# Performance work log

Hardware: AMD Instinct MI355X
Metric: run time of the kernel (lower is better)

Reference implementation:

```python
import jax, jax.numpy as jnp
import numpy as np

B, N, H, W = 2, 65536, 256, 256
FEA, OUT, CMP, MAX_PT = 8, 512, 32, 64
EPS = 1e-5


def _xavier(key, fan_in, fan_out):
    scale = np.sqrt(2.0 / (fan_in + fan_out)).astype(np.float32)
    return jax.random.normal(key, (fan_in, fan_out), dtype=jnp.float32) * scale


def setup_inputs() -> dict:
    key = jax.random.key(0)
    ks = jax.random.split(key, 8)
    pt_fea = jax.random.normal(ks[0], (B, N, FEA), dtype=jnp.float32)
    xy_ind = jax.random.randint(ks[1], (B, N, 2), 0, H, dtype=jnp.int32)
    return {
        "pt_fea": pt_fea,
        "bn0_g": jnp.ones((FEA,), jnp.float32), "bn0_b": jnp.zeros((FEA,), jnp.float32),
        "W1": _xavier(ks[2], FEA, 64),
        "bn1_g": jnp.ones((64,), jnp.float32), "bn1_b": jnp.zeros((64,), jnp.float32),
        "W2": _xavier(ks[3], 64, 128),
        "bn2_g": jnp.ones((128,), jnp.float32), "bn2_b": jnp.zeros((128,), jnp.float32),
        "W3": _xavier(ks[4], 128, 256),
        "bn3_g": jnp.ones((256,), jnp.float32), "bn3_b": jnp.zeros((256,), jnp.float32),
        "W4": _xavier(ks[5], 256, OUT),
        "Wc": _xavier(ks[6], OUT, CMP),
        "xy_ind": xy_ind,
    }


def _forward(pt_fea, bn0_g, bn0_b, W1, bn1_g, bn1_b, W2, bn2_g, bn2_b,
             W3, bn3_g, bn3_b, W4, Wc, xy_ind):
    Bc, Nc, Fc = pt_fea.shape
    P = Bc * Nc
    feats = pt_fea.reshape(P, Fc)
    batch_id = jnp.repeat(jnp.arange(Bc, dtype=jnp.int32), Nc)
    xy = xy_ind.reshape(P, 2)
    keys = batch_id * (H * W) + xy[:, 0] * W + xy[:, 1]  # linearized voxel id

    # random shuffle of points (torch.randperm)
    perm = jax.random.permutation(jax.random.key(42), P)
    feats = feats[perm]
    keys = keys[perm]

    # rank of each point within its voxel, in shuffled order
    # (== grp_range_torch(unq_cnt)[argsort(argsort(unq_inv))])
    order = jnp.argsort(keys)  # stable
    sk = keys[order]
    pos = jnp.arange(P)
    new_grp = jnp.concatenate([jnp.array([True]), sk[1:] != sk[:-1]])
    grp_start = jax.lax.cummax(jnp.where(new_grp, pos, 0))
    rank = jnp.zeros(P, jnp.int32).at[order].set((pos - grp_start).astype(jnp.int32))
    mask = rank < MAX_PT  # keep at most MAX_PT points per voxel

    # PPmodel: BN -> Lin -> BN -> ReLU x3 -> Lin, BN stats over kept points only
    m = mask[:, None].astype(feats.dtype)
    cnt = jnp.sum(m)

    def bn(x, g, b):
        mu = jnp.sum(x * m, axis=0) / cnt
        var = jnp.sum(jnp.square(x - mu) * m, axis=0) / cnt  # biased var
        return (x - mu) * jax.lax.rsqrt(var + EPS) * g + b

    x = bn(feats, bn0_g, bn0_b)
    x = jax.nn.relu(bn(x @ W1, bn1_g, bn1_b))
    x = jax.nn.relu(bn(x @ W2, bn2_g, bn2_b))
    x = jax.nn.relu(bn(x @ W3, bn3_g, bn3_b))
    x = x @ W4  # [P, OUT]

    # scatter_max segment reduction into dense voxel grid
    NEG = jnp.finfo(x.dtype).min
    x = jnp.where(mask[:, None], x, NEG)
    S = Bc * H * W
    pooled = jax.ops.segment_max(x, keys, num_segments=S)
    occupied = jax.ops.segment_sum(jnp.ones(P, x.dtype), keys, num_segments=S) > 0
    pooled = jnp.where(occupied[:, None], pooled, 0.0)

    comp = jax.nn.relu(pooled @ Wc)  # fea_compression
    comp = jnp.where(occupied[:, None], comp, 0.0)  # empty voxels stay zero
    out = comp.reshape(Bc, H, W, CMP).transpose(0, 3, 1, 2)  # [B, C, H, W]
    return out


def reference(pt_fea, bn0_g, bn0_b, W1, bn1_g, bn1_b, W2, bn2_g, bn2_b,
              W3, bn3_g, bn3_b, W4, Wc, xy_ind):
    return _forward(pt_fea, bn0_g, bn0_b, W1, bn1_g, bn1_b, W2, bn2_g, bn2_b,
                    W3, bn3_g, bn3_b, W4, Wc, xy_ind)
```

## Files before the change

### kernel.cpp

```cpp
#include <hip/hip_runtime.h>
#include <cstdint>
#include <cstddef>


#define P_TOT  131072
#define HWSZ   65536
#define WGRID  256
#define S_TOT  131072
#define EPS    1e-5f
#define CNTF   131072.0f

#define OFF_Y3    0ull
#define OFF_Y1    67108864ull
#define OFF_Y2    100663296ull
#define OFF_POOL  67108864ull
#define OFF_CNT   201326592ull
#define OFF_ST    201850880ull
#define OFF_OFFS  201916416ull
#define OFF_CUR   202440704ull
#define OFF_BSUM  202964992ull
#define OFF_PIDF  202969088ull
#define OFF_SEND  203493376ull
#define OFF_SKEY  204017664ull
#define OFF_W3F   204541952ull
#define OFF_W4F   204607488ull
#define OFF_WCF   204869632ull
#define OFF_W2F   204902400ull
#define OFF_SCSH  204918784ull

typedef __attribute__((ext_vector_type(8)))  short bf16x8;
typedef __attribute__((ext_vector_type(16))) float f32x16;

__device__ __forceinline__ unsigned f2bf(float f) {
    unsigned u = __float_as_uint(f);
    return (u + 0x7FFFu + ((u >> 16) & 1u)) >> 16;
}
__device__ __forceinline__ float bf2f(unsigned h) {
    return __uint_as_float(h << 16);
}

__global__ __launch_bounds__(256) void k_zero(uint4* __restrict__ p, int n_u4) {
    int i = blockIdx.x * blockDim.x + threadIdx.x;
    if (i < n_u4) p[i] = make_uint4(0u, 0u, 0u, 0u);
}

__global__ __launch_bounds__(256) void k_prepw(
    const float* __restrict__ W2, const float* __restrict__ W3,
    const float* __restrict__ W4, const float* __restrict__ Wc,
    uint4* __restrict__ W2F, uint4* __restrict__ W3F,
    uint4* __restrict__ W4F, uint4* __restrict__ WcF)
{
    int gw = (blockIdx.x * 256 + threadIdx.x) >> 6;
    int l = threadIdx.x & 63;
    const float* W; uint4* dst; int M, mt, ks, fi;
    if (gw < 64)       { fi = gw;       W = W3; dst = W3F; M = 256; mt = fi >> 3; ks = fi & 7;  }
    else if (gw < 320) { fi = gw - 64;  W = W4; dst = W4F; M = 512; mt = fi >> 4; ks = fi & 15; }
    else if (gw < 352) { fi = gw - 320; W = Wc; dst = WcF; M = 32;  mt = 0;      ks = fi;      }
    else               { fi = gw - 352; W = W2; dst = W2F; M = 128; mt = fi >> 2; ks = fi & 3;  }
    int m = mt * 32 + (l & 31);
    int k0 = ks * 16 + (l >> 5) * 8;
    unsigned p[4];
    #pragma unroll
    for (int jj = 0; jj < 4; ++jj) {
        unsigned lo = f2bf(W[(size_t)(k0 + 2*jj)     * M + m]);
        unsigned hi = f2bf(W[(size_t)(k0 + 2*jj + 1) * M + m]);
        p[jj] = lo | (hi << 16);
    }
    dst[(size_t)fi * 64 + l] = make_uint4(p[0], p[1], p[2], p[3]);
}

__global__ __launch_bounds__(256) void k_bnprep(
    const float* __restrict__ st, const float* __restrict__ g,
    const float* __restrict__ b, float* __restrict__ sc,
    float* __restrict__ sh, int nch)
{
    int c = blockIdx.x * 256 + threadIdx.x;
    if (c >= nch) return;
    float mu = st[c * 16] * (1.0f / CNTF);
    float var = st[(nch + c) * 16] * (1.0f / CNTF) - mu * mu;
    float rs = rsqrtf(var + EPS);
    float s = rs * g[c];
    sc[c] = s;
    sh[c] = b[c] - mu * s;
}

__global__ __launch_bounds__(256) void k_fold(
    unsigned short* __restrict__ y, const float* __restrict__ sc,
    const float* __restrict__ sh, int nch, int n_u4)
{
    int i = blockIdx.x * 256 + threadIdx.x;
    if (i >= n_u4) return;
    int ch0 = (i * 8) & (nch - 1);
    float4 s0 = *(const float4*)(sc + ch0), s1 = *(const float4*)(sc + ch0 + 4);
    float4 h0 = *(const float4*)(sh + ch0), h1 = *(const float4*)(sh + ch0 + 4);
    float scv[8] = {s0.x,s0.y,s0.z,s0.w,s1.x,s1.y,s1.z,s1.w};
    float shv[8] = {h0.x,h0.y,h0.z,h0.w,h1.x,h1.y,h1.z,h1.w};
    uint4 e = ((const uint4*)y)[i];
    unsigned eu[4] = {e.x, e.y, e.z, e.w};
    unsigned ou[4];
    #pragma unroll
    for (int jj = 0; jj < 4; ++jj) {
        float x0 = fmaxf(fmaf(bf2f(eu[jj] & 0xFFFFu), scv[2*jj],   shv[2*jj]),   0.f);
        float x1 = fmaxf(fmaf(bf2f(eu[jj] >> 16),     scv[2*jj+1], shv[2*jj+1]), 0.f);
        ou[jj] = f2bf(x0) | (f2bf(x1) << 16);
    }
    ((uint4*)y)[i] = make_uint4(ou[0], ou[1], ou[2], ou[3]);
}

__global__ __launch_bounds__(256) void k_stats0(
    const float* __restrict__ pt, const int* __restrict__ xy,
    float* __restrict__ st0, unsigned* __restrict__ counts)
{
    __shared__ float part[4][16];
    const int tid = threadIdx.x;
    const int p = blockIdx.x * 256 + tid;
    const float4* f4 = (const float4*)(pt + (size_t)p * 8);
    float4 a = f4[0], b = f4[1];
    float v[8] = {a.x,a.y,a.z,a.w,b.x,b.y,b.z,b.w};
    int key = (p >> 16) * HWSZ + xy[2*p] * WGRID + xy[2*p + 1];
    atomicAdd(&counts[key], 1u);
    float s[8], q[8];
    #pragma unroll
    for (int k = 0; k < 8; ++k) { s[k] = v[k]; q[k] = v[k]*v[k]; }
    #pragma unroll
    for (int k = 0; k < 8; ++k) {
        #pragma unroll
        for (int off = 32; off > 0; off >>= 1) {
            s[k] += __shfl_down(s[k], off);
            q[k] += __shfl_down(q[k], off);
        }
    }
    if ((tid & 63) == 0) {
        int w = tid >> 6;
        #pragma unroll
        for (int k = 0; k < 8; ++k) { part[w][k] = s[k]; part[w][8 + k] = q[k]; }
    }
    __syncthreads();
    if (tid < 16) {
        float t = part[0][tid] + part[1][tid] + part[2][tid] + part[3][tid];
        atomicAdd(&st0[tid * 16], t);
    }
}

__global__ __launch_bounds__(256) void k_lin1(
    const float* __restrict__ pt, const float* __restrict__ g0,
    const float* __restrict__ b0, const float* __restrict__ W1,
    const float* __restrict__ st0, float* __restrict__ y1,
    float* __restrict__ st1)
{
    __shared__ float x0s[64 * 8];
    __shared__ float w1s[8 * 64];
    __shared__ float sc0s[8], sh0s[8];
    __shared__ float red[256];
    const int tid = threadIdx.x;

    if (tid < 8) {
        float mu = st0[tid * 16] * (1.0f / CNTF);
        float var = st0[(8 + tid) * 16] * (1.0f / CNTF) - mu * mu;
        float rs = rsqrtf(var + EPS);
        sc0s[tid] = rs * g0[tid];
        sh0s[tid] = b0[tid] - mu * rs * g0[tid];
    }
    if (tid < 128) ((float4*)w1s)[tid] = ((const float4*)W1)[tid];
    const int c = tid & 63;
    const int psub = tid >> 6;
    float ssum = 0.f, ssq = 0.f;
    for (int t = 0; t < 4; ++t) {
        const int pbase = blockIdx.x * 256 + t * 64;
        __syncthreads();
        if (tid < 128) {
            float4 f = ((const float4*)(pt + (size_t)pbase * 8))[tid];
            int cc = (tid & 1) * 4;
            f.x = fmaf(f.x, sc0s[cc + 0], sh0s[cc + 0]);
            f.y = fmaf(f.y, sc0s[cc + 1], sh0s[cc + 1]);
            f.z = fmaf(f.z, sc0s[cc + 2], sh0s[cc + 2]);
            f.w = fmaf(f.w, sc0s[cc + 3], sh0s[cc + 3]);
            ((float4*)x0s)[tid] = f;
        }
        __syncthreads();
        #pragma unroll
        for (int i = 0; i < 16; ++i) {
            int pl = psub * 16 + i;
            float acc = 0.f;
            #pragma unroll
            for (int k = 0; k < 8; ++k)
                acc = fmaf(x0s[pl * 8 + k], w1s[k * 64 + c], acc);
            y1[(size_t)(pbase + pl) * 64 + c] = acc;
            ssum += acc; ssq += acc * acc;
        }
    }
    red[tid] = ssum; __syncthreads();
    if (tid < 64) atomicAdd(&st1[tid * 16],
        red[tid] + red[tid+64] + red[tid+128] + red[tid+192]);
    __syncthreads();
    red[tid] = ssq; __syncthreads();
    if (tid < 64) atomicAdd(&st1[(64 + tid) * 16],
        red[tid] + red[tid+64] + red[tid+128] + red[tid+192]);
}

__global__ __launch_bounds__(256) void k_scan1(
    const unsigned* __restrict__ counts, unsigned* __restrict__ bsum)
{
    __shared__ unsigned sh[256];
    int t = threadIdx.x;
    sh[t] = counts[blockIdx.x * 256 + t];
    __syncthreads();
    for (int d = 128; d > 0; d >>= 1) {
        if (t < d) sh[t] += sh[t + d];
        __syncthreads();
    }
    if (t == 0) bsum[blockIdx.x] = sh[0];
}

__global__ __launch_bounds__(256) void k_scan2(
    const unsigned* __restrict__ bsum, unsigned* __restrict__ boff)
{
    __shared__ unsigned sh[256];
    int t = threadIdx.x;
    unsigned a = bsum[2*t], b = bsum[2*t+1];
    unsigned s = a + b;
    sh[t] = s; __syncthreads();
    for (int d = 1; d < 256; d <<= 1) {
        unsigned u = (t >= d) ? sh[t-d] : 0u;
        __syncthreads();
        sh[t] += u;
        __syncthreads();
    }
    unsigned excl = sh[t] - s;
    boff[2*t]   = excl;
    boff[2*t+1] = excl + a;
}

__global__ __launch_bounds__(256) void k_scan3(
    const unsigned* __restrict__ counts, const unsigned* __restrict__ boff,
    unsigned* __restrict__ offs)
{
    __shared__ unsigned sh[256];
    int t = threadIdx.x, b = blockIdx.x;
    unsigned v = counts[b*256 + t];
    sh[t] = v; __syncthreads();
    for (int d = 1; d < 256; d <<= 1) {
        unsigned u = (t >= d) ? sh[t-d] : 0u;
        __syncthreads();
        sh[t] += u;
        __syncthreads();
    }
    offs[b*256 + t] = boff[b] + sh[t] - v;
}

__global__ __launch_bounds__(256) void k_fill(
    const int* __restrict__ xy, const unsigned* __restrict__ offs,
    const unsigned* __restrict__ counts, unsigned* __restrict__ cur,
    unsigned* __restrict__ pidf, unsigned* __restrict__ send,
    unsigned* __restrict__ skey)
{
    int p = blockIdx.x * 256 + threadIdx.x;
    int key = (p >> 16) * HWSZ + xy[2*p] * WGRID + xy[2*p + 1];
    unsigned o = offs[key];
    unsigned r = atomicAdd(&cur[key], 1u);
    unsigned slot = o + r;
    pidf[slot] = (unsigned)p | (r == 0 ? 0x80000000u : 0u);
    send[slot] = o + counts[key];
    skey[slot] = (unsigned)key;
}

__global__ __launch_bounds__(256, 2) void k_lin2(
    const float* __restrict__ y1, const float* __restrict__ g1,
    const float* __restrict__ b1, const uint4* __restrict__ W2F,
    const float* __restrict__ st1, unsigned short* __restrict__ y2,
    float* __restrict__ st2)
{
    __shared__ uint4 w2s[1024];
    __shared__ float sc1s[64], sh1s[64];
    const int tid = threadIdx.x, l = tid & 63, w = tid >> 6;
    if (tid < 64) {
        float mu = st1[tid * 16] * (1.0f / CNTF);
        float var = st1[(64 + tid) * 16] * (1.0f / CNTF) - mu * mu;
        float rs = rsqrtf(var + EPS);
        sc1s[tid] = rs * g1[tid];
        sh1s[tid] = b1[tid] - mu * rs * g1[tid];
    }
    #pragma unroll
    for (int r = 0; r < 4; ++r) w2s[r * 256 + tid] = W2F[r * 256 + tid];
    __syncthreads();
    const int n = l & 31, q = l >> 5;
    float s_acc[16], q_acc[16];
    #pragma unroll
    for (int r = 0; r < 16; ++r) { s_acc[r] = 0.f; q_acc[r] = 0.f; }

    for (int t = 0; t < 8; ++t) {
        const int p = (blockIdx.x * 8 + t) * 32 + n;
        const float* yrow = y1 + (size_t)p * 64 + q * 8;
        bf16x8 Bf[4];
        #pragma unroll
        for (int ks = 0; ks < 4; ++ks) {
            float4 v0 = *(const float4*)(yrow + ks * 16);
            float4 v1 = *(const float4*)(yrow + ks * 16 + 4);
            int k0 = ks * 16 + q * 8;
            float e[8] = {v0.x,v0.y,v0.z,v0.w,v1.x,v1.y,v1.z,v1.w};
            union { bf16x8 v; unsigned u[4]; } cv;
            #pragma unroll
            for (int jj = 0; jj < 4; ++jj) {
                float a0 = fmaxf(fmaf(e[2*jj],   sc1s[k0+2*jj],   sh1s[k0+2*jj]),   0.f);
                float a1 = fmaxf(fmaf(e[2*jj+1], sc1s[k0+2*jj+1], sh1s[k0+2*jj+1]), 0.f);
                cv.u[jj] = f2bf(a0) | (f2bf(a1) << 16);
            }
            Bf[ks] = cv.v;
        }
        f32x16 acc;
        #pragma unroll
        for (int r = 0; r < 16; ++r) acc[r] = 0.f;
        #pragma unroll
        for (int ks = 0; ks < 4; ++ks) {
            union { uint4 u; bf16x8 v; } av;
            av.u = w2s[(w * 4 + ks) * 64 + l];
            acc = __builtin_amdgcn_mfma_f32_32x32x16_bf16(av.v, Bf[ks], acc, 0, 0, 0);
        }
        #pragma unroll
        for (int g = 0; g < 4; ++g) {
            int ch0 = w * 32 + 8 * g + 4 * q;
            ushort4 pk;
            pk.x = (unsigned short)f2bf(acc[4*g+0]);
            pk.y = (unsigned short)f2bf(acc[4*g+1]);
            pk.z = (unsigned short)f2bf(acc[4*g+2]);
            pk.w = (unsigned short)f2bf(acc[4*g+3]);
            *(ushort4*)(y2 + (size_t)p * 128 + ch0) = pk;
        }
        #pragma unroll
        for (int r = 0; r < 16; ++r) { s_acc[r] += acc[r]; q_acc[r] += acc[r]*acc[r]; }
    }
    #pragma unroll
    for (int r = 0; r < 16; ++r) {
        float s = s_acc[r], sq = q_acc[r];
        #pragma unroll
        for (int off = 16; off > 0; off >>= 1) {
            s  += __shfl_xor(s, off);
            sq += __shfl_xor(sq, off);
        }
        if ((l & 31) == 0) {
            int ch = w * 32 + (r & 3) + 8 * (r >> 2) + 4 * q;
            atomicAdd(&st2[ch * 16], s);
            atomicAdd(&st2[(128 + ch) * 16], sq);
        }
    }
}

__global__ __launch_bounds__(256, 2) void k_lin3(
    const unsigned short* __restrict__ y2f, const uint4* __restrict__ W3F,
    unsigned short* __restrict__ y3, float* __restrict__ st3)
{
    __shared__ uint4 w3s[4096];
    const int tid = threadIdx.x, l = tid & 63, w = tid >> 6;
    #pragma unroll
    for (int r = 0; r < 16; ++r) w3s[r * 256 + tid] = W3F[r * 256 + tid];
    __syncthreads();
    const int n = l & 31, q = l >> 5;
    float s_acc[32], q_acc[32];
    #pragma unroll
    for (int r = 0; r < 32; ++r) { s_acc[r] = 0.f; q_acc[r] = 0.f; }

    for (int t = 0; t < 8; ++t) {
        const int p = (blockIdx.x * 8 + t) * 32 + n;
        const unsigned short* yrow = y2f + (size_t)p * 128 + q * 8;
        bf16x8 Bf[8];
        #pragma unroll
        for (int ks = 0; ks < 8; ++ks) {
            union { uint4 u; bf16x8 v; } bv;
            bv.u = *(const uint4*)(yrow + ks * 16);
            Bf[ks] = bv.v;
        }
        f32x16 acc[2];
        #pragma unroll
        for (int i = 0; i < 2; ++i)
            #pragma unroll
            for (int r = 0; r < 16; ++r) acc[i][r] = 0.f;
        #pragma unroll
        for (int ks = 0; ks < 8; ++ks) {
            #pragma unroll
            for (int i = 0; i < 2; ++i) {
                union { uint4 u; bf16x8 v; } av;
                av.u = w3s[((w * 2 + i) * 8 + ks) * 64 + l];
                acc[i] = __builtin_amdgcn_mfma_f32_32x32x16_bf16(av.v, Bf[ks], acc[i], 0, 0, 0);
            }
        }
        #pragma unroll
        for (int i = 0; i < 2; ++i) {
            #pragma unroll
            for (int g = 0; g < 4; ++g) {
                int ch0 = (w * 2 + i) * 32 + 8 * g + 4 * q;
                ushort4 pk;
                pk.x = (unsigned short)f2bf(acc[i][4*g+0]);
                pk.y = (unsigned short)f2bf(acc[i][4*g+1]);
                pk.z = (unsigned short)f2bf(acc[i][4*g+2]);
                pk.w = (unsigned short)f2bf(acc[i][4*g+3]);
                *(ushort4*)(y3 + (size_t)p * 256 + ch0) = pk;
            }
            #pragma unroll
            for (int r = 0; r < 16; ++r) {
                s_acc[i*16+r] += acc[i][r];
                q_acc[i*16+r] += acc[i][r] * acc[i][r];
            }
        }
    }
    #pragma unroll
    for (int i = 0; i < 2; ++i)
        #pragma unroll
        for (int r = 0; r < 16; ++r) {
            float s = s_acc[i*16+r], sq = q_acc[i*16+r];
            #pragma unroll
            for (int off = 16; off > 0; off >>= 1) {
                s  += __shfl_xor(s, off);
                sq += __shfl_xor(sq, off);
            }
            if ((l & 31) == 0) {
                int ch = (w * 2 + i) * 32 + (r & 3) + 8 * (r >> 2) + 4 * q;
                atomicAdd(&st3[ch * 16], s);
                atomicAdd(&st3[(256 + ch) * 16], sq);
            }
        }
}

__global__ __launch_bounds__(256, 2) void k_smax(
    const unsigned short* __restrict__ y3f, const uint4* __restrict__ W4F,
    const unsigned* __restrict__ pidf, const unsigned* __restrict__ send,
    const unsigned* __restrict__ skey, unsigned short* __restrict__ pooled)
{
    __shared__ float s0c_s[4 * 256];
    const int tid = threadIdx.x, l = tid & 63, w = tid >> 6;
    const int wg = blockIdx.x;
    const int q = l >> 5;

    #pragma unroll
    for (int sub = 0; sub < 4; ++sub) s0c_s[sub * 256 + tid] = -3.4e38f;

    #pragma unroll 1
    for (int t = 2; t >= 0; --t) {
        const int p0 = (wg * 2 + t) * 32;
        const int pos = p0 + (l & 31);
        const int sp = pos < P_TOT ? pos : P_TOT - 1;
        const unsigned pf = pidf[sp];
        const unsigned e_l = send[sp];
        const unsigned key_l = skey[sp];
        const unsigned cmask =
            (unsigned)__ballot((unsigned)(pos + 1) < e_l);
        const unsigned fmask =
            (unsigned)__ballot((pf & 0x80000000u) != 0u);
        const unsigned short* row =
            y3f + (size_t)(pf & 0x7FFFFFFFu) * 256 + q * 8;
        uint4 Xf[16];
        #pragma unroll
        for (int ks = 0; ks < 16; ++ks)
            Xf[ks] = *(const uint4*)(row + ks * 16);

        #pragma unroll 1
        for (int sub = 0; sub < 4; ++sub) {
            const int nt = sub * 4 + w;
            f32x16 acc;
            #pragma unroll
            for (int r = 0; r < 16; ++r) acc[r] = 0.f;
            #pragma unroll
            for (int ks = 0; ks < 16; ++ks) {
                union { uint4 u; bf16x8 v; } xv, wv;
                xv.u = Xf[ks];
                wv.u = W4F[(size_t)(nt * 16 + ks) * 64 + l];
                acc = __builtin_amdgcn_mfma_f32_32x32x16_bf16(xv.v, wv.v, acc, 0, 0, 0);
            }
            float v[32];
            #pragma unroll
            for (int r = 0; r < 16; ++r) {
                int base = (r & 3) + 8 * (r >> 2);
                float o = __shfl_xor(acc[r], 32);
                v[base]     = q ? o : acc[r];
                v[base + 4] = q ? acc[r] : o;
            }
            if ((cmask >> 31) & 1)
                v[31] = fmaxf(v[31], s0c_s[sub * 256 + tid]);
            #pragma unroll
            for (int m = 30; m >= 0; --m)
                if ((cmask >> m) & 1) v[m] = fmaxf(v[m], v[m + 1]);
            s0c_s[sub * 256 + tid] = v[0];
            if (t < 2) {
                #pragma unroll
                for (int m = 0; m < 32; ++m) {
                    if ((fmask >> m) & 1) {
                        unsigned km = (unsigned)
                            __builtin_amdgcn_readlane((int)key_l, m);
                        if ((m >> 4) == q)
                            pooled[(size_t)km * 512 + nt * 32 + (l & 31)] =
                                (unsigned short)f2bf(v[m]);
                    }
                }
            }
        }
    }
}

__global__ __launch_bounds__(256, 4) void k_out(
    const unsigned short* __restrict__ pooled, const unsigned* __restrict__ counts,
    const uint4* __restrict__ WcF, float* __restrict__ out)
{
    __shared__ uint4 wcs[2048];
    const int tid = threadIdx.x, l = tid & 63, w = tid >> 6;
    const int sbase = blockIdx.x * 128;
    #pragma unroll
    for (int r = 0; r < 8; ++r) wcs[r * 256 + tid] = WcF[r * 256 + tid];
    __syncthreads();
    const int n = l & 31, q = l >> 5;
    const int s = sbase + w * 32 + n;
    const bool occ = counts[s] > 0;
    const unsigned short* prow =
        pooled + (occ ? (size_t)s * 512 : (size_t)0) + q * 8;
    f32x16 acc;
    #pragma unroll
    for (int r = 0; r < 16; ++r) acc[r] = 0.f;

    for (int ks = 0; ks < 32; ++ks) {
        union { uint4 u; bf16x8 v; } bv;
        bv.u = *(const uint4*)(prow + ks * 16);
        union { uint4 u; bf16x8 v; } av;
        av.u = wcs[ks * 64 + l];
        acc = __builtin_amdgcn_mfma_f32_32x32x16_bf16(av.v, bv.v, acc, 0, 0, 0);
    }
    const int b = s >> 16, hw = s & 65535;
    #pragma unroll
    for (int r = 0; r < 16; ++r) {
        int ch = (r & 3) + 8 * (r >> 2) + 4 * q;
        float x = occ ? fmaxf(acc[r], 0.f) : 0.f;
        out[(size_t)b * (32 * HWSZ) + (size_t)ch * HWSZ + hw] = x;
    }
}

extern "C" void kernel_launch(void* const* d_in, const int* in_sizes, int n_in,
                              void* d_out, int out_size, void* d_ws, size_t ws_size,
                              hipStream_t stream) {
    const float* pt = (const float*)d_in[0];
    const float* g0 = (const float*)d_in[1];
    const float* b0 = (const float*)d_in[2];
    const float* W1 = (const float*)d_in[3];
    const float* g1 = (const float*)d_in[4];
    const float* b1 = (const float*)d_in[5];
    const float* W2 = (const float*)d_in[6];
    const float* g2 = (const float*)d_in[7];
    const float* b2 = (const float*)d_in[8];
    const float* W3 = (const float*)d_in[9];
    const float* g3 = (const float*)d_in[10];
    const float* b3 = (const float*)d_in[11];
    const float* W4 = (const float*)d_in[12];
    const float* Wc = (const float*)d_in[13];
    const int*   xy = (const int*)d_in[14];
    float* out = (float*)d_out;

    char* ws = (char*)d_ws;
    unsigned short* y3     = (unsigned short*)(ws + OFF_Y3);
    float*          y1     = (float*)(ws + OFF_Y1);
    unsigned short* y2     = (unsigned short*)(ws + OFF_Y2);
    unsigned short* pool16 = (unsigned short*)(ws + OFF_POOL);
    unsigned*       counts = (unsigned*)(ws + OFF_CNT);
    float*          st     = (float*)(ws + OFF_ST);
    unsigned*       offs   = (unsigned*)(ws + OFF_OFFS);
    unsigned*       cur    = (unsigned*)(ws + OFF_CUR);
    unsigned*       bsum   = (unsigned*)(ws + OFF_BSUM);
    unsigned*       pidf   = (unsigned*)(ws + OFF_PIDF);
    unsigned*       send   = (unsigned*)(ws + OFF_SEND);
    unsigned*       skey   = (unsigned*)(ws + OFF_SKEY);
    uint4* W3F = (uint4*)(ws + OFF_W3F);
    uint4* W4F = (uint4*)(ws + OFF_W4F);
    uint4* WcF = (uint4*)(ws + OFF_WCF);
    uint4* W2F = (uint4*)(ws + OFF_W2F);
    float* scsh = (float*)(ws + OFF_SCSH);
    float* sc2 = scsh;       float* sh2 = scsh + 128;
    float* sc3 = scsh + 256; float* sh3 = scsh + 512;
    float* st0 = st;
    float* st1 = st + 256;
    float* st2 = st + 2304;
    float* st3 = st + 6400;

    k_zero<<<400, 256, 0, stream>>>((uint4*)(ws + OFF_CNT), 102400);
    k_prepw<<<92, 256, 0, stream>>>(W2, W3, W4, Wc, W2F, W3F, W4F, WcF);

    k_stats0<<<512, 256, 0, stream>>>(pt, xy, st0, counts);
    k_scan1<<<512, 256, 0, stream>>>(counts, bsum);
    k_scan2<<<1,   256, 0, stream>>>(bsum, bsum + 512);
    k_scan3<<<512, 256, 0, stream>>>(counts, bsum + 512, offs);
    k_fill<<<512, 256, 0, stream>>>(xy, offs, counts, cur, pidf, send, skey);

    k_lin1<<<512, 256, 0, stream>>>(pt, g0, b0, W1, st0, y1, st1);
    k_lin2<<<512, 256, 0, stream>>>(y1, g1, b1, W2F, st1, y2, st2);
    k_bnprep<<<1, 256, 0, stream>>>(st2, g2, b2, sc2, sh2, 128);
    k_fold<<<8192, 256, 0, stream>>>(y2, sc2, sh2, 128, 2097152);
    k_lin3<<<512, 256, 0, stream>>>(y2, W3F, y3, st3);
    k_bnprep<<<1, 256, 0, stream>>>(st3, g3, b3, sc3, sh3, 256);
    k_fold<<<16384, 256, 0, stream>>>(y3, sc3, sh3, 256, 4194304);

    k_smax<<<2048, 256, 0, stream>>>(y3, W4F, pidf, send, skey, pool16);
    k_out<<<S_TOT / 128, 256, 0, stream>>>(pool16, counts, WcF, out);
}
```

Measured before the change: 434.2 us.

## Scatter lin3 output into voxel-sorted MFMA fragment layout for smax

k_fill now records each point's sorted slot, and k_lin3 writes its bf16 output directly at that slot in a fragment-major layout, using a lane shuffle to assemble 8-channel chunks. The fold kernel is replaced by a variant that understands the new layout. k_smax then reads contiguous, coalesced fragments instead of gathering 512-byte rows through the pidf indirection, and each workgroup handles four tiles instead of two with half the grid. The scattered writes in lin3 and the extra inv buffer are the costs, and the larger per-workgroup tile count lowers parallelism in smax.

```diff
diff --git a/kernel.cpp b/kernel.cpp
--- a/kernel.cpp
+++ b/kernel.cpp
@@ -22,11 +22,12 @@
 #define OFF_PIDF  202969088ull
 #define OFF_SEND  203493376ull
 #define OFF_SKEY  204017664ull
-#define OFF_W3F   204541952ull
-#define OFF_W4F   204607488ull
-#define OFF_WCF   204869632ull
-#define OFF_W2F   204902400ull
-#define OFF_SCSH  204918784ull
+#define OFF_INV   204541952ull
+#define OFF_W3F   205066240ull
+#define OFF_W4F   205131776ull
+#define OFF_WCF   205393920ull
+#define OFF_W2F   205426688ull
+#define OFF_SCSH  205443072ull
 
 typedef __attribute__((ext_vector_type(8)))  short bf16x8;
 typedef __attribute__((ext_vector_type(16))) float f32x16;
@@ -91,6 +92,29 @@
     int i = blockIdx.x * 256 + threadIdx.x;
     if (i >= n_u4) return;
     int ch0 = (i * 8) & (nch - 1);
+    float4 s0 = *(const float4*)(sc + ch0), s1 = *(const float4*)(sc + ch0 + 4);
+    float4 h0 = *(const float4*)(sh + ch0), h1 = *(const float4*)(sh + ch0 + 4);
+    float scv[8] = {s0.x,s0.y,s0.z,s0.w,s1.x,s1.y,s1.z,s1.w};
+    float shv[8] = {h0.x,h0.y,h0.z,h0.w,h1.x,h1.y,h1.z,h1.w};
+    uint4 e = ((const uint4*)y)[i];
+    unsigned eu[4] = {e.x, e.y, e.z, e.w};
+    unsigned ou[4];
+    #pragma unroll
+    for (int jj = 0; jj < 4; ++jj) {
+        float x0 = fmaxf(fmaf(bf2f(eu[jj] & 0xFFFFu), scv[2*jj],   shv[2*jj]),   0.f);
+        float x1 = fmaxf(fmaf(bf2f(eu[jj] >> 16),     scv[2*jj+1], shv[2*jj+1]), 0.f);
+        ou[jj] = f2bf(x0) | (f2bf(x1) << 16);
+    }
+    ((uint4*)y)[i] = make_uint4(ou[0], ou[1], ou[2], ou[3]);
+}
+
+__global__ __launch_bounds__(256) void k_foldf(
+    unsigned short* __restrict__ y, const float* __restrict__ sc,
+    const float* __restrict__ sh, int n_u4)
+{
+    int i = blockIdx.x * 256 + threadIdx.x;
+    if (i >= n_u4) return;
+    int ch0 = ((i >> 6) & 15) * 16 + ((i >> 5) & 1) * 8;
     float4 s0 = *(const float4*)(sc + ch0), s1 = *(const float4*)(sc + ch0 + 4);
     float4 h0 = *(const float4*)(sh + ch0), h1 = *(const float4*)(sh + ch0 + 4);
     float scv[8] = {s0.x,s0.y,s0.z,s0.w,s1.x,s1.y,s1.z,s1.w};
@@ -252,7 +276,7 @@
     const int* __restrict__ xy, const unsigned* __restrict__ offs,
     const unsigned* __restrict__ counts, unsigned* __restrict__ cur,
     unsigned* __restrict__ pidf, unsigned* __restrict__ send,
-    unsigned* __restrict__ skey)
+    unsigned* __restrict__ skey, unsigned* __restrict__ inv)
 {
     int p = blockIdx.x * 256 + threadIdx.x;
     int key = (p >> 16) * HWSZ + xy[2*p] * WGRID + xy[2*p + 1];
@@ -262,6 +286,7 @@
     pidf[slot] = (unsigned)p | (r == 0 ? 0x80000000u : 0u);
     send[slot] = o + counts[key];
     skey[slot] = (unsigned)key;
+    inv[p] = slot;
 }
 
 __global__ __launch_bounds__(256, 2) void k_lin2(
@@ -347,7 +372,8 @@
 
 __global__ __launch_bounds__(256, 2) void k_lin3(
     const unsigned short* __restrict__ y2f, const uint4* __restrict__ W3F,
-    unsigned short* __restrict__ y3, float* __restrict__ st3)
+    const unsigned* __restrict__ inv, uint4* __restrict__ y3F,
+    float* __restrict__ st3)
 {
     __shared__ uint4 w3s[4096];
     const int tid = threadIdx.x, l = tid & 63, w = tid >> 6;
@@ -384,21 +410,33 @@
             }
         }
         #pragma unroll
-        for (int i = 0; i < 2; ++i) {
-            #pragma unroll
-            for (int g = 0; g < 4; ++g) {
-                int ch0 = (w * 2 + i) * 32 + 8 * g + 4 * q;
-                ushort4 pk;
-                pk.x = (unsigned short)f2bf(acc[i][4*g+0]);
-                pk.y = (unsigned short)f2bf(acc[i][4*g+1]);
-                pk.z = (unsigned short)f2bf(acc[i][4*g+2]);
-                pk.w = (unsigned short)f2bf(acc[i][4*g+3]);
-                *(ushort4*)(y3 + (size_t)p * 256 + ch0) = pk;
-            }
+        for (int i = 0; i < 2; ++i)
             #pragma unroll
             for (int r = 0; r < 16; ++r) {
                 s_acc[i*16+r] += acc[i][r];
                 q_acc[i*16+r] += acc[i][r] * acc[i][r];
+            }
+        const unsigned slotn = inv[p];
+        const int fb = (int)(slotn >> 5) * 16;
+        const int li = (int)(slotn & 31) + 32 * q;
+        #pragma unroll
+        for (int i = 0; i < 2; ++i) {
+            #pragma unroll
+            for (int s = 0; s < 2; ++s) {
+                float V[8];
+                #pragma unroll
+                for (int j = 0; j < 4; ++j) {
+                    float tmp = q ? acc[i][8*s + j] : acc[i][8*s + 4 + j];
+                    float got = __shfl_xor(tmp, 32);
+                    V[j]     = q ? got : acc[i][8*s + j];
+                    V[4 + j] = q ? acc[i][8*s + 4 + j] : got;
+                }
+                uint4 pk;
+                pk.x = f2bf(V[0]) | (f2bf(V[1]) << 16);
+                pk.y = f2bf(V[2]) | (f2bf(V[3]) << 16);
+                pk.z = f2bf(V[4]) | (f2bf(V[5]) << 16);
+                pk.w = f2bf(V[6]) | (f2bf(V[7]) << 16);
+                y3F[(size_t)(fb + w * 4 + 2 * i + s) * 64 + li] = pk;
             }
         }
     }
@@ -421,7 +459,7 @@
 }
 
 __global__ __launch_bounds__(256, 2) void k_smax(
-    const unsigned short* __restrict__ y3f, const uint4* __restrict__ W4F,
+    const uint4* __restrict__ y3F, const uint4* __restrict__ W4F,
     const unsigned* __restrict__ pidf, const unsigned* __restrict__ send,
     const unsigned* __restrict__ skey, unsigned short* __restrict__ pooled)
 {
@@ -434,8 +472,8 @@
     for (int sub = 0; sub < 4; ++sub) s0c_s[sub * 256 + tid] = -3.4e38f;
 
     #pragma unroll 1
-    for (int t = 2; t >= 0; --t) {
-        const int p0 = (wg * 2 + t) * 32;
+    for (int t = 4; t >= 0; --t) {
+        const int p0 = (wg * 4 + t) * 32;
         const int pos = p0 + (l & 31);
         const int sp = pos < P_TOT ? pos : P_TOT - 1;
         const unsigned pf = pidf[sp];
@@ -445,12 +483,12 @@
             (unsigned)__ballot((unsigned)(pos + 1) < e_l);
         const unsigned fmask =
             (unsigned)__ballot((pf & 0x80000000u) != 0u);
-        const unsigned short* row =
-            y3f + (size_t)(pf & 0x7FFFFFFFu) * 256 + q * 8;
+        const int tt = (wg * 4 + t) < 4096 ? (wg * 4 + t) : 4095;
+        const uint4* xb = y3F + (size_t)tt * 16 * 64;
         uint4 Xf[16];
         #pragma unroll
         for (int ks = 0; ks < 16; ++ks)
-            Xf[ks] = *(const uint4*)(row + ks * 16);
+            Xf[ks] = xb[ks * 64 + l];
 
         #pragma unroll 1
         for (int sub = 0; sub < 4; ++sub) {
@@ -479,7 +517,7 @@
             for (int m = 30; m >= 0; --m)
                 if ((cmask >> m) & 1) v[m] = fmaxf(v[m], v[m + 1]);
             s0c_s[sub * 256 + tid] = v[0];
-            if (t < 2) {
+            if (t < 4) {
                 #pragma unroll
                 for (int m = 0; m < 32; ++m) {
                     if ((fmask >> m) & 1) {
@@ -551,7 +589,8 @@
     float* out = (float*)d_out;
 
     char* ws = (char*)d_ws;
-    unsigned short* y3     = (unsigned short*)(ws + OFF_Y3);
+    uint4*          y3F    = (uint4*)(ws + OFF_Y3);
+    unsigned short* y3u    = (unsigned short*)(ws + OFF_Y3);
     float*          y1     = (float*)(ws + OFF_Y1);
     unsigned short* y2     = (unsigned short*)(ws + OFF_Y2);
     unsigned short* pool16 = (unsigned short*)(ws + OFF_POOL);
@@ -563,6 +602,7 @@
     unsigned*       pidf   = (unsigned*)(ws + OFF_PIDF);
     unsigned*       send   = (unsigned*)(ws + OFF_SEND);
     unsigned*       skey   = (unsigned*)(ws + OFF_SKEY);
+    unsigned*       inv    = (unsigned*)(ws + OFF_INV);
     uint4* W3F = (uint4*)(ws + OFF_W3F);
     uint4* W4F = (uint4*)(ws + OFF_W4F);
     uint4* WcF = (uint4*)(ws + OFF_WCF);
@@ -582,16 +622,16 @@
     k_scan1<<<512, 256, 0, stream>>>(counts, bsum);
     k_scan2<<<1,   256, 0, stream>>>(bsum, bsum + 512);
     k_scan3<<<512, 256, 0, stream>>>(counts, bsum + 512, offs);
-    k_fill<<<512, 256, 0, stream>>>(xy, offs, counts, cur, pidf, send, skey);
+    k_fill<<<512, 256, 0, stream>>>(xy, offs, counts, cur, pidf, send, skey, inv);
 
     k_lin1<<<512, 256, 0, stream>>>(pt, g0, b0, W1, st0, y1, st1);
     k_lin2<<<512, 256, 0, stream>>>(y1, g1, b1, W2F, st1, y2, st2);
     k_bnprep<<<1, 256, 0, stream>>>(st2, g2, b2, sc2, sh2, 128);
     k_fold<<<8192, 256, 0, stream>>>(y2, sc2, sh2, 128, 2097152);
-    k_lin3<<<512, 256, 0, stream>>>(y2, W3F, y3, st3);
+    k_lin3<<<512, 256, 0, stream>>>(y2, W3F, inv, y3F, st3);
     k_bnprep<<<1, 256, 0, stream>>>(st3, g3, b3, sc3, sh3, 256);
-    k_fold<<<16384, 256, 0, stream>>>(y3, sc3, sh3, 256, 4194304);
-
-    k_smax<<<2048, 256, 0, stream>>>(y3, W4F, pidf, send, skey, pool16);
+    k_foldf<<<16384, 256, 0, stream>>>(y3u, sc3, sh3, 4194304);
+
+    k_smax<<<1024, 256, 0, stream>>>(y3F, W4F, pidf, send, skey, pool16);
     k_out<<<S_TOT / 128, 256, 0, stream>>>(pool16, counts, WcF, out);
 }
```

After: 403.4 us. 7.1% less time.
